# Performance work log

Measured on AMD Instinct MI355X. Metric: run time of the kernel, lower is better.

## Reference

```python
import jax, jax.numpy as jnp
import numpy as np
from jax import lax

T, B, I, H = 32768, 1, 128, 512  # seq_len, batch(=1 due to squeeze(1)), input_dim, hidden_dim
HEAD = 25

def setup_inputs() -> dict:
    key = jax.random.key(0)
    ks = jax.random.split(key, 8)
    s = 1.0 / np.sqrt(H)  # pytorch LSTM init scale
    return {
        "x": jax.random.normal(ks[0], (T, B, I), dtype=jnp.float32),
        "W_ih": jax.random.uniform(ks[1], (4 * H, I), jnp.float32, -s, s),
        "W_hh": jax.random.uniform(ks[2], (4 * H, H), jnp.float32, -s, s),
        "b_ih": jax.random.uniform(ks[3], (4 * H,), jnp.float32, -s, s),
        "b_hh": jax.random.uniform(ks[4], (4 * H,), jnp.float32, -s, s),
        "W1": jax.random.uniform(ks[5], (HEAD, H), jnp.float32, -s, s),
        "b1": jax.random.uniform(ks[6], (HEAD,), jnp.float32, -s, s),
        "Wout": jax.random.uniform(ks[7], (1, HEAD), jnp.float32, -s, s),
    }

def reference(x, W_ih, W_hh, b_ih, b_hh, W1, b1, Wout):
    # Precompute input projections for all timesteps (one big GEMM): [T, B, 4H]
    xg = jnp.einsum('tbi,gi->tbg', x, W_ih) + (b_ih + b_hh)

    def step(carry, xg_t):
        h, c = carry  # [B, H] each
        gates = xg_t + h @ W_hh.T  # [B, 4H]
        i_g, f_g, g_g, o_g = jnp.split(gates, 4, axis=-1)  # pytorch gate order i,f,g,o
        i = jax.nn.sigmoid(i_g)
        f = jax.nn.sigmoid(f_g)
        g = jnp.tanh(g_g)
        o = jax.nn.sigmoid(o_g)
        c = f * c + i * g
        h = o * jnp.tanh(c)
        return (h, c), h

    h0 = jnp.zeros((B, H), x.dtype)
    _, hs = lax.scan(step, (h0, h0), xg)  # hs: [T, B, H]

    hid = hs[:, 0, :]  # h_1.squeeze(1) -> [T, H]
    # forward applies c1 then out (c2 is defined but unused in the original)
    out = (hid @ W1.T + b1) @ Wout.T  # [T, 1]
    return out
```

## Files before the change

kernel.cpp:

```cpp
#include <hip/hip_runtime.h>
#include <math.h>


#define T_SEQ 32768
#define HID   512
#define INP   128
#define NWG   32
#define NTH   512
#define HSL   16
#define KW    64
#define KX    16
#define NPK   256

typedef unsigned long long u64;
typedef unsigned int u32;

__device__ __forceinline__ float fast_sigmoid(float x) {
    return 1.0f / (1.0f + __expf(-x));
}
__device__ __forceinline__ float fast_tanh(float x) {
    float a = fabsf(x);
    float e = __expf(-2.0f * a);
    float r = (1.0f - e) / (1.0f + e);
    return copysignf(r, x);
}

__global__ void __launch_bounds__(NTH, 1) lstm_persist(
    const float* __restrict__ x,
    const float* __restrict__ W_ih,
    const float* __restrict__ W_hh,
    const float* __restrict__ b_ih,
    const float* __restrict__ b_hh,
    const float* __restrict__ W1,
    const float* __restrict__ b1,
    const float* __restrict__ Wout,
    u64* __restrict__ hbuf,
    float* __restrict__ out)
{
    const int w   = blockIdx.x;
    const int tid = threadIdx.x;
    const int wv  = tid >> 6;
    const int l   = tid & 63;
    const int rw  = l >> 3;
    const int j   = l & 7;
    const int g   = rw >> 1;
    const int b   = rw & 1;
    const bool is_out = (w == 0 && wv == 1);

    __shared__ __align__(16) float h_lds[2][HID];
    __shared__ u64 gather_lds[8];

    const int grow = g * HID + w * HSL + 2 * wv + b;

    float wr[KW], wi[KX];
#pragma unroll
    for (int kk = 0; kk < 16; ++kk) {
        const int p = (kk + 2 * j) & 15;
        const float4 v4 = *(const float4*)&W_hh[grow * HID + j * KW + 4 * p];
        wr[4 * kk + 0] = v4.x; wr[4 * kk + 1] = v4.y;
        wr[4 * kk + 2] = v4.z; wr[4 * kk + 3] = v4.w;
    }
#pragma unroll
    for (int k = 0; k < KX; k += 4) {
        const float4 v4 = *(const float4*)&W_ih[grow * INP + j * KX + k];
        wi[k] = v4.x; wi[k + 1] = v4.y; wi[k + 2] = v4.z; wi[k + 3] = v4.w;
    }
    float brow = b_ih[grow] + b_hh[grow];

    float weff_o[8];
    float be = 0.0f;
#pragma unroll
    for (int i = 0; i < 8; ++i) weff_o[i] = 0.0f;
    if (is_out) {
#pragma unroll
        for (int i = 0; i < 8; ++i) {
            float s = 0.0f;
            for (int p = 0; p < 25; ++p) s += Wout[p] * W1[p * HID + l + 64 * i];
            weff_o[i] = s;
        }
        for (int p = 0; p < 25; ++p) be += b1[p] * Wout[p];
    }
#pragma unroll
    for (int k = 0; k < KW; ++k) asm volatile("" : "+v"(wr[k]));
#pragma unroll
    for (int k = 0; k < KX; ++k) asm volatile("" : "+v"(wi[k]));
#pragma unroll
    for (int i = 0; i < 8; ++i) asm volatile("" : "+v"(weff_o[i]));
    asm volatile("" : "+v"(brow));
    asm volatile("" : "+v"(be));

    float c = 0.0f;
    float xa[KX];
#pragma unroll
    for (int k = 0; k < KX; ++k) xa[k] = x[j * KX + k];

    bool dead = false;

    for (u32 t = 0; t <= T_SEQ; ++t) {
        if (t == T_SEQ && w != 0) break;

        float xd0 = 0.0f, xd1 = 0.0f, xd2 = 0.0f, xd3 = 0.0f;
#pragma unroll
        for (int k = 0; k < KX; k += 4) {
            xd0 += wi[k + 0] * xa[k + 0];
            xd1 += wi[k + 1] * xa[k + 1];
            xd2 += wi[k + 2] * xa[k + 2];
            xd3 += wi[k + 3] * xa[k + 3];
        }
        const int tn = (t + 1 < T_SEQ) ? (int)(t + 1) : (T_SEQ - 1);
        if (wv != 0) {
#pragma unroll
            for (int k = 0; k < KX; k += 4) {
                const float4 x4 = *(const float4*)&x[tn * INP + j * KX + k];
                xa[k + 0] = x4.x; xa[k + 1] = x4.y;
                xa[k + 2] = x4.z; xa[k + 3] = x4.w;
            }
        }

        if (wv == 0 && !dead) {
            const u64* P = hbuf + (t & 1) * NPK;
            float2* HL = (float2*)h_lds[t & 1];
            bool mine = false;
            int guard = 0;
            while (true) {
                if (!mine) {
                    u64 pr[4];
                    bool ok = true;
#pragma unroll
                    for (int i = 0; i < 4; ++i) {
                        pr[i] = __hip_atomic_load(&P[l + 64 * i],
                                                  __ATOMIC_RELAXED,
                                                  __HIP_MEMORY_SCOPE_AGENT);
                        ok = ok && ((((u32)pr[i]) ^ t) & 15u) == 0u;
                    }
                    if (ok) {
#pragma unroll
                        for (int i = 0; i < 4; ++i) {
                            float2 hp;
                            hp.x = __uint_as_float((u32)pr[i]);
                            hp.y = __uint_as_float((u32)(pr[i] >> 32));
                            HL[l + 64 * i] = hp;
                        }
                        mine = true;
                    }
                }
                if (__ballot(mine) == ~0ull) break;
                if (++guard > (1 << 22)) { dead = true; break; }
            }
        }
        __syncthreads();

        if (t < T_SEQ) {
            float a0 = xd0, a1 = xd1, a2 = xd2, a3 = xd3;
            const float4* hl4 = (const float4*)&h_lds[t & 1][j * KW];
#pragma unroll
            for (int kk = 0; kk < 16; ++kk) {
                const int p = (kk + 2 * j) & 15;
                const float4 h4 = hl4[p];
                a0 += wr[4 * kk + 0] * h4.x;
                a1 += wr[4 * kk + 1] * h4.y;
                a2 += wr[4 * kk + 2] * h4.z;
                a3 += wr[4 * kk + 3] * h4.w;
            }
            if (wv == 0) {
#pragma unroll
                for (int k = 0; k < KX; k += 4) {
                    const float4 x4 = *(const float4*)&x[tn * INP + j * KX + k];
                    xa[k + 0] = x4.x; xa[k + 1] = x4.y;
                    xa[k + 2] = x4.z; xa[k + 3] = x4.w;
                }
            }
            float acc = (a0 + a1) + (a2 + a3);
            acc += __shfl_xor(acc, 1);
            acc += __shfl_xor(acc, 2);
            acc += __shfl_xor(acc, 4);
            acc += brow;
            const float ig = acc;
            const float fg = __shfl(acc, l + 16);
            const float gg = __shfl(acc, l + 32);
            const float og = __shfl(acc, l + 48);
            const float iv = fast_sigmoid(ig);
            const float fv = fast_sigmoid(fg);
            const float gv = fast_tanh(gg);
            const float ov = fast_sigmoid(og);
            c = fv * c + iv * gv;
            const float hv = ov * fast_tanh(c);
            const float hv1 = __shfl(hv, 8);
            if (l == 0) {
                const u32 b0 = (__float_as_uint(hv) & ~15u) | ((t + 1) & 15u);
                const u32 b1v = __float_as_uint(hv1);
                gather_lds[wv] = ((u64)b1v << 32) | (u64)b0;
            }
            __syncthreads();
            if (wv == 0 && l < 8) {
                __hip_atomic_store(&hbuf[((t + 1) & 1) * NPK + w * 8 + l],
                                   gather_lds[l],
                                   __ATOMIC_RELAXED, __HIP_MEMORY_SCOPE_AGENT);
            }
        }

        if (is_out && t >= 1) {
            float pd = 0.0f;
#pragma unroll
            for (int i = 0; i < 8; ++i)
                pd += h_lds[t & 1][l + 64 * i] * weff_o[i];
            pd += __shfl_xor(pd, 1);
            pd += __shfl_xor(pd, 2);
            pd += __shfl_xor(pd, 4);
            pd += __shfl_xor(pd, 8);
            pd += __shfl_xor(pd, 16);
            pd += __shfl_xor(pd, 32);
            if (l == 0) out[t - 1] = pd + be;
        }
    }
}

extern "C" void kernel_launch(void* const* d_in, const int* in_sizes, int n_in,
                              void* d_out, int out_size, void* d_ws, size_t ws_size,
                              hipStream_t stream)
{
    const float* x    = (const float*)d_in[0];
    const float* W_ih = (const float*)d_in[1];
    const float* W_hh = (const float*)d_in[2];
    const float* b_ih = (const float*)d_in[3];
    const float* b_hh = (const float*)d_in[4];
    const float* W1   = (const float*)d_in[5];
    const float* b1   = (const float*)d_in[6];
    const float* Wout = (const float*)d_in[7];
    float* out = (float*)d_out;

    u64* hbuf = (u64*)d_ws;

    hipMemsetAsync(d_ws, 0, 2 * NPK * sizeof(u64), stream);
    lstm_persist<<<NWG, NTH, 0, stream>>>(x, W_ih, W_hh, b_ih, b_hh, W1, b1,
                                          Wout, hbuf, out);
}
```

Before: 65.56 ms.

## Halve workgroups to 16, each thread computing two gate rows

Cuts the persistent LSTM grid from 32 to 16 workgroups. Each thread now holds W_hh and W_ih weights for two gate rows (i/f and g/o pairs), so each workgroup produces 32 hidden units per step and publishes 16 packed words. The goal is to lower the cost of the per-step cross-workgroup barrier, with fewer producers to poll and less global traffic. In exchange each step does twice the serial FMA work per thread and needs roughly twice the register file for weights.

```diff
diff --git a/kernel.cpp b/kernel.cpp
--- a/kernel.cpp
+++ b/kernel.cpp
@@ -5,9 +5,8 @@
 #define T_SEQ 32768
 #define HID   512
 #define INP   128
-#define NWG   32
+#define NWG   16
 #define NTH   512
-#define HSL   16
 #define KW    64
 #define KX    16
 #define NPK   256
@@ -43,29 +42,37 @@
     const int l   = tid & 63;
     const int rw  = l >> 3;
     const int j   = l & 7;
-    const int g   = rw >> 1;
-    const int b   = rw & 1;
+    const int b   = rw & 3;
+    const int gg  = rw >> 2;
     const bool is_out = (w == 0 && wv == 1);
 
     __shared__ __align__(16) float h_lds[2][HID];
-    __shared__ u64 gather_lds[8];
-
-    const int grow = g * HID + w * HSL + 2 * wv + b;
-
-    float wr[KW], wi[KX];
+    __shared__ u64 gather_lds[16];
+
+    const int e_glob = 32 * w + 4 * wv + b;
+    const int grow0 = (2 * gg + 0) * HID + e_glob;
+    const int grow1 = (2 * gg + 1) * HID + e_glob;
+
+    float wr0[KW], wr1[KW], wi0[KX], wi1[KX];
 #pragma unroll
     for (int kk = 0; kk < 16; ++kk) {
         const int p = (kk + 2 * j) & 15;
-        const float4 v4 = *(const float4*)&W_hh[grow * HID + j * KW + 4 * p];
-        wr[4 * kk + 0] = v4.x; wr[4 * kk + 1] = v4.y;
-        wr[4 * kk + 2] = v4.z; wr[4 * kk + 3] = v4.w;
+        const float4 v0 = *(const float4*)&W_hh[grow0 * HID + j * KW + 4 * p];
+        wr0[4 * kk + 0] = v0.x; wr0[4 * kk + 1] = v0.y;
+        wr0[4 * kk + 2] = v0.z; wr0[4 * kk + 3] = v0.w;
+        const float4 v1 = *(const float4*)&W_hh[grow1 * HID + j * KW + 4 * p];
+        wr1[4 * kk + 0] = v1.x; wr1[4 * kk + 1] = v1.y;
+        wr1[4 * kk + 2] = v1.z; wr1[4 * kk + 3] = v1.w;
     }
 #pragma unroll
     for (int k = 0; k < KX; k += 4) {
-        const float4 v4 = *(const float4*)&W_ih[grow * INP + j * KX + k];
-        wi[k] = v4.x; wi[k + 1] = v4.y; wi[k + 2] = v4.z; wi[k + 3] = v4.w;
-    }
-    float brow = b_ih[grow] + b_hh[grow];
+        const float4 v0 = *(const float4*)&W_ih[grow0 * INP + j * KX + k];
+        wi0[k] = v0.x; wi0[k + 1] = v0.y; wi0[k + 2] = v0.z; wi0[k + 3] = v0.w;
+        const float4 v1 = *(const float4*)&W_ih[grow1 * INP + j * KX + k];
+        wi1[k] = v1.x; wi1[k + 1] = v1.y; wi1[k + 2] = v1.z; wi1[k + 3] = v1.w;
+    }
+    float brow0 = b_ih[grow0] + b_hh[grow0];
+    float brow1 = b_ih[grow1] + b_hh[grow1];
 
     float weff_o[8];
     float be = 0.0f;
@@ -81,12 +88,15 @@
         for (int p = 0; p < 25; ++p) be += b1[p] * Wout[p];
     }
 #pragma unroll
-    for (int k = 0; k < KW; ++k) asm volatile("" : "+v"(wr[k]));
-#pragma unroll
-    for (int k = 0; k < KX; ++k) asm volatile("" : "+v"(wi[k]));
+    for (int k = 0; k < KW; ++k) { asm volatile("" : "+v"(wr0[k]));
+                                   asm volatile("" : "+v"(wr1[k])); }
+#pragma unroll
+    for (int k = 0; k < KX; ++k) { asm volatile("" : "+v"(wi0[k]));
+                                   asm volatile("" : "+v"(wi1[k])); }
 #pragma unroll
     for (int i = 0; i < 8; ++i) asm volatile("" : "+v"(weff_o[i]));
-    asm volatile("" : "+v"(brow));
+    asm volatile("" : "+v"(brow0));
+    asm volatile("" : "+v"(brow1));
     asm volatile("" : "+v"(be));
 
     float c = 0.0f;
@@ -99,13 +109,13 @@
     for (u32 t = 0; t <= T_SEQ; ++t) {
         if (t == T_SEQ && w != 0) break;
 
-        float xd0 = 0.0f, xd1 = 0.0f, xd2 = 0.0f, xd3 = 0.0f;
-#pragma unroll
-        for (int k = 0; k < KX; k += 4) {
-            xd0 += wi[k + 0] * xa[k + 0];
-            xd1 += wi[k + 1] * xa[k + 1];
-            xd2 += wi[k + 2] * xa[k + 2];
-            xd3 += wi[k + 3] * xa[k + 3];
+        float p0a = 0.0f, p0b = 0.0f, p1a = 0.0f, p1b = 0.0f;
+#pragma unroll
+        for (int k = 0; k < KX; k += 2) {
+            p0a += wi0[k + 0] * xa[k + 0];
+            p0b += wi0[k + 1] * xa[k + 1];
+            p1a += wi1[k + 0] * xa[k + 0];
+            p1b += wi1[k + 1] * xa[k + 1];
         }
         const int tn = (t + 1 < T_SEQ) ? (int)(t + 1) : (T_SEQ - 1);
         if (wv != 0) {
@@ -151,16 +161,17 @@
         __syncthreads();
 
         if (t < T_SEQ) {
-            float a0 = xd0, a1 = xd1, a2 = xd2, a3 = xd3;
+            float a0 = p0a + p0b, a1 = p1a + p1b;
+            float q0 = 0.0f, q1 = 0.0f;
             const float4* hl4 = (const float4*)&h_lds[t & 1][j * KW];
 #pragma unroll
             for (int kk = 0; kk < 16; ++kk) {
                 const int p = (kk + 2 * j) & 15;
                 const float4 h4 = hl4[p];
-                a0 += wr[4 * kk + 0] * h4.x;
-                a1 += wr[4 * kk + 1] * h4.y;
-                a2 += wr[4 * kk + 2] * h4.z;
-                a3 += wr[4 * kk + 3] * h4.w;
+                a0 += wr0[4 * kk + 0] * h4.x + wr0[4 * kk + 1] * h4.y;
+                q0 += wr0[4 * kk + 2] * h4.z + wr0[4 * kk + 3] * h4.w;
+                a1 += wr1[4 * kk + 0] * h4.x + wr1[4 * kk + 1] * h4.y;
+                q1 += wr1[4 * kk + 2] * h4.z + wr1[4 * kk + 3] * h4.w;
             }
             if (wv == 0) {
 #pragma unroll
@@ -170,30 +181,38 @@
                     xa[k + 2] = x4.z; xa[k + 3] = x4.w;
                 }
             }
-            float acc = (a0 + a1) + (a2 + a3);
-            acc += __shfl_xor(acc, 1);
-            acc += __shfl_xor(acc, 2);
-            acc += __shfl_xor(acc, 4);
-            acc += brow;
-            const float ig = acc;
-            const float fg = __shfl(acc, l + 16);
-            const float gg = __shfl(acc, l + 32);
-            const float og = __shfl(acc, l + 48);
-            const float iv = fast_sigmoid(ig);
-            const float fv = fast_sigmoid(fg);
-            const float gv = fast_tanh(gg);
-            const float ov = fast_sigmoid(og);
+            float acc0 = a0 + q0, acc1 = a1 + q1;
+            acc0 += __shfl_xor(acc0, 1);
+            acc1 += __shfl_xor(acc1, 1);
+            acc0 += __shfl_xor(acc0, 2);
+            acc1 += __shfl_xor(acc1, 2);
+            acc0 += __shfl_xor(acc0, 4);
+            acc1 += __shfl_xor(acc1, 4);
+            acc0 += brow0;
+            acc1 += brow1;
+            const float gG = __shfl(acc0, l + 32);
+            const float oG = __shfl(acc1, l + 32);
+            const float iv = fast_sigmoid(acc0);
+            const float fv = fast_sigmoid(acc1);
+            const float gv = fast_tanh(gG);
+            const float ov = fast_sigmoid(oG);
             c = fv * c + iv * gv;
             const float hv = ov * fast_tanh(c);
-            const float hv1 = __shfl(hv, 8);
+            const float h0 = __shfl(hv, 0);
+            const float h1 = __shfl(hv, 8);
+            const float h2 = __shfl(hv, 16);
+            const float h3 = __shfl(hv, 24);
             if (l == 0) {
-                const u32 b0 = (__float_as_uint(hv) & ~15u) | ((t + 1) & 15u);
-                const u32 b1v = __float_as_uint(hv1);
-                gather_lds[wv] = ((u64)b1v << 32) | (u64)b0;
+                const u32 t0 = (__float_as_uint(h0) & ~15u) | ((t + 1) & 15u);
+                const u32 t2 = (__float_as_uint(h2) & ~15u) | ((t + 1) & 15u);
+                gather_lds[2 * wv + 0] =
+                    ((u64)__float_as_uint(h1) << 32) | (u64)t0;
+                gather_lds[2 * wv + 1] =
+                    ((u64)__float_as_uint(h3) << 32) | (u64)t2;
             }
             __syncthreads();
-            if (wv == 0 && l < 8) {
-                __hip_atomic_store(&hbuf[((t + 1) & 1) * NPK + w * 8 + l],
+            if (wv == 0 && l < 16) {
+                __hip_atomic_store(&hbuf[((t + 1) & 1) * NPK + w * 16 + l],
                                    gather_lds[l],
                                    __ATOMIC_RELAXED, __HIP_MEMORY_SCOPE_AGENT);
             }
```

New measurement: 142.6 ms. 118% more time.
